# Kernel optimization log

Hardware: AMD Instinct MI355X
Metric: run time of the kernel (lower is better)

The kernel has to match this reference:

```python
import jax, jax.numpy as jnp
import numpy as np

N = 50000   # nodes
E = 800000  # edges (avg degree 16)
IN, H, OUT = 128, 128, 64


def setup_inputs() -> dict:
    key = jax.random.key(0)
    ks = jax.random.split(key, 8)

    def w(k, shape):
        fan_in = shape[0]
        return (jax.random.normal(k, shape, jnp.float32) / np.float32(np.sqrt(fan_in)))

    x = jax.random.normal(ks[0], (N, IN), jnp.float32)
    edge_index = jax.random.randint(ks[1], (2, E), 0, N, jnp.int64)
    return {
        "x": x,
        "edge_index": edge_index,
        "W1": w(ks[2], (IN, H)), "b1": jnp.zeros((H,), jnp.float32),
        "W2": w(ks[3], (H, H)),  "b2": jnp.zeros((H,), jnp.float32),
        "W3": w(ks[4], (H, H)),  "b3": jnp.zeros((H,), jnp.float32),
        "Wd1": w(ks[5], (H, H)), "bd1": jnp.zeros((H,), jnp.float32),
        "Wd2": w(ks[6], (H, OUT)), "bd2": jnp.zeros((OUT,), jnp.float32),
    }


def _gcn_conv(x, src, dst, norm, W, b):
    # x: [N, Cin] -> linear transform, gather along edges, normalized scatter-add
    h = x @ W                                   # [N, Cout]
    msg = h[src] * norm[:, None]                # [E+N, Cout]
    out = jax.ops.segment_sum(msg, dst, num_segments=N)
    return out + b


def reference(x, edge_index, W1, b1, W2, b2, W3, b3, Wd1, bd1, Wd2, bd2):
    # Add self-loops (PyG GCNConv default) and compute symmetric normalization.
    loops = jnp.arange(N, dtype=edge_index.dtype)
    src = jnp.concatenate([edge_index[0], loops])   # [E+N]
    dst = jnp.concatenate([edge_index[1], loops])   # [E+N]
    deg = jax.ops.segment_sum(jnp.ones_like(dst, dtype=x.dtype), dst, num_segments=N)
    dinv = jnp.where(deg > 0, jax.lax.rsqrt(deg), jnp.zeros_like(deg))
    norm = dinv[src] * dinv[dst]                    # [E+N]

    h = jax.nn.relu(_gcn_conv(x, src, dst, norm, W1, b1))
    h = jax.nn.relu(_gcn_conv(h, src, dst, norm, W2, b2))
    h = jax.nn.relu(_gcn_conv(h, src, dst, norm, W3, b3))

    h = jax.nn.relu(h @ Wd1 + bd1)
    return jax.nn.sigmoid(h @ Wd2 + bd2)            # [N, OUT]
```

## Files before the change

kernel.cpp:

```cpp
#include <hip/hip_runtime.h>
#include <hip/hip_bf16.h>
#include <hip/hip_fp16.h>

#define N_NODES 50000
#define N_EDGES 800000
#define C_H 128
#define C_OUT 64
#define NBLK 196
#define TSTRIDE 136
#define E_PAD 950272
#define MM_BLKS 782

typedef __attribute__((ext_vector_type(8))) short bf16x8;
typedef __attribute__((ext_vector_type(4))) float f32x4;

static __device__ __forceinline__ float bf_lo(unsigned int u) { return __uint_as_float(u << 16); }
static __device__ __forceinline__ float bf_hi(unsigned int u) { return __uint_as_float(u & 0xffff0000u); }
static __device__ __forceinline__ unsigned short f2bf(float f) {
    __hip_bfloat16 h = __float2bfloat16(f);
    return *(unsigned short*)&h;
}
static __device__ __forceinline__ unsigned int pack2(float a, float b) {
    return (unsigned int)f2bf(a) | ((unsigned int)f2bf(b) << 16);
}
static __device__ __forceinline__ unsigned short f2h_bits(float f) {
    union { __half h; unsigned short u; } c; c.h = __float2half_rn(f); return c.u;
}
static __device__ __forceinline__ float h_bits2f(unsigned short u) {
    union { __half h; unsigned short u; } c; c.u = u; return __half2float(c.h);
}

__global__ void prep_kernel(const int* __restrict__ dst, int* __restrict__ counts,
                            int* __restrict__ rank,
                            const float* __restrict__ W1, const float* __restrict__ W2,
                            const float* __restrict__ W3, const float* __restrict__ Wd1,
                            const float* __restrict__ Wd2,
                            unsigned short* __restrict__ P1, unsigned short* __restrict__ P2,
                            unsigned short* __restrict__ P3, unsigned short* __restrict__ Pd1,
                            unsigned short* __restrict__ Pd2,
                            unsigned int* __restrict__ epay) {
    int b = blockIdx.x;
    if (b < 3125) {
        int e = b * 256 + threadIdx.x;
        rank[e] = atomicAdd(&counts[dst[e]], 1);
    } else if (b < 3413) {
        int idx = (b - 3125) * 256 + threadIdx.x;
        if (idx < 4 * 16384) {
            int which = idx >> 14;
            int r = idx & 16383;
            const float* W = (which == 0) ? W1 : (which == 1) ? W2 : (which == 2) ? W3 : Wd1;
            unsigned short* P = (which == 0) ? P1 : (which == 1) ? P2 : (which == 2) ? P3 : Pd1;
            int j = r & 7, lane = (r >> 3) & 63, t = r >> 9;
            int nb = t & 7, kb = t >> 3;
            int k = kb * 32 + ((lane >> 4) << 3) + j;
            int n = nb * 16 + (lane & 15);
            P[r] = f2bf(W[(size_t)k * 128 + n]);
        } else {
            int r = idx - 65536;
            if (r < 8192) {
                int j = r & 7, lane = (r >> 3) & 63, t = r >> 9;
                int nb = t & 3, kb = t >> 2;
                int k = kb * 32 + ((lane >> 4) << 3) + j;
                int n = nb * 16 + (lane & 15);
                Pd2[r] = f2bf(Wd2[(size_t)k * 64 + n]);
            }
        }
    } else {
        int i = (b - 3413) * 256 + threadIdx.x;
        *(uint4*)(epay + (size_t)i * 4) = make_uint4(0, 0, 0, 0);
    }
}

__global__ void __launch_bounds__(256) scan_fused_kernel(
        const int* __restrict__ counts, int* __restrict__ bsum, int* __restrict__ bo,
        int* __restrict__ ctr_flag, float* __restrict__ dinv, int* __restrict__ rowptr) {
    __shared__ int ws[4];
    __shared__ int ws2[4];
    __shared__ int sLast;
    const int b = blockIdx.x;
    const int i = b * 256 + threadIdx.x;
    const int lane = threadIdx.x & 63, w = threadIdx.x >> 6;

    int v = (i < N_NODES) ? counts[i] : 0;
    if (i < N_NODES) dinv[i] = rsqrtf((float)v + 1.0f);
    int vp = (v + 3) & ~3;
    int x = vp;
    #pragma unroll
    for (int off = 1; off < 64; off <<= 1) {
        int t = __shfl_up(x, off, 64);
        if (lane >= off) x += t;
    }
    if (lane == 63) ws[w] = x;
    __syncthreads();
    if (threadIdx.x == 0) {
        int run = 0;
        #pragma unroll
        for (int k = 0; k < 4; ++k) { int t = ws[k]; ws[k] = run; run += t; }
        bsum[b] = run;
    }
    __syncthreads();
    int excl_local = x - vp + ws[w];

    if (threadIdx.x == 0) {
        __threadfence();
        int old = __hip_atomic_fetch_add(&ctr_flag[0], 1, __ATOMIC_ACQ_REL, __HIP_MEMORY_SCOPE_AGENT);
        sLast = (old == NBLK - 1) ? 1 : 0;
    }
    __syncthreads();
    if (sLast) {
        int j = threadIdx.x;
        int bv = (j < NBLK) ? bsum[j] : 0;
        int y = bv;
        #pragma unroll
        for (int off = 1; off < 64; off <<= 1) {
            int t = __shfl_up(y, off, 64);
            if (lane >= off) y += t;
        }
        if (lane == 63) ws2[w] = y;
        __syncthreads();
        if (j == 0) {
            int run = 0;
            #pragma unroll
            for (int k = 0; k < 4; ++k) { int t = ws2[k]; ws2[k] = run; run += t; }
        }
        __syncthreads();
        int be = y - bv + ws2[w];
        if (j < NBLK) bo[j] = be;
        if (j == 255) rowptr[N_NODES] = be + bv;
        __syncthreads();
        if (j == 0) {
            __threadfence();
            __hip_atomic_store(&ctr_flag[1], 1, __ATOMIC_RELEASE, __HIP_MEMORY_SCOPE_AGENT);
        }
    }
    if (threadIdx.x == 0) {
        while (__hip_atomic_load(&ctr_flag[1], __ATOMIC_ACQUIRE, __HIP_MEMORY_SCOPE_AGENT) == 0) {}
    }
    __syncthreads();
    if (i < N_NODES) rowptr[i] = excl_local + bo[b];
}

__global__ void __launch_bounds__(256) fill_mm_kernel(
        const float* __restrict__ x, const unsigned short* __restrict__ P1,
        unsigned short* __restrict__ XW1,
        const int* __restrict__ src, const int* __restrict__ dst,
        const float* __restrict__ dinv,
        const int* __restrict__ rowptr, const int* __restrict__ rank,
        unsigned int* __restrict__ epay) {
    int b = blockIdx.x;
    if (b < MM_BLKS) {
        const int lane = threadIdx.x & 63;
        const int wave = threadIdx.x >> 6;
        const int wid  = b * 4 + wave;
        if (wid * 16 >= N_NODES) return;
        const int node = wid * 16 + (lane & 15);
        const int quad = lane >> 4;
        f32x4 acc[8];
        #pragma unroll
        for (int nb = 0; nb < 8; ++nb) acc[nb] = (f32x4){0.f, 0.f, 0.f, 0.f};
        #pragma unroll
        for (int kb = 0; kb < 4; ++kb) {
            const float* p = x + (size_t)node * 128 + kb * 32 + quad * 8;
            float4 lo = *(const float4*)p;
            float4 hi = *(const float4*)(p + 4);
            union { bf16x8 v; unsigned int u[4]; } tmp;
            tmp.u[0] = pack2(lo.x, lo.y); tmp.u[1] = pack2(lo.z, lo.w);
            tmp.u[2] = pack2(hi.x, hi.y); tmp.u[3] = pack2(hi.z, hi.w);
            #pragma unroll
            for (int nb = 0; nb < 8; ++nb) {
                bf16x8 wf = *(const bf16x8*)(P1 + ((size_t)(kb * 8 + nb) * 64 + lane) * 8);
                acc[nb] = __builtin_amdgcn_mfma_f32_16x16x32_bf16(wf, tmp.v, acc[nb], 0, 0, 0);
            }
        }
        #pragma unroll
        for (int nb = 0; nb < 8; ++nb) {
            int ch = nb * 16 + quad * 4;
            uint2 o;
            o.x = pack2(acc[nb][0], acc[nb][1]);
            o.y = pack2(acc[nb][2], acc[nb][3]);
            *(uint2*)(XW1 + (size_t)node * C_H + ch) = o;
        }
    } else {
        int e = (b - MM_BLKS) * 256 + threadIdx.x;
        if (e < N_EDGES) {
            int d = dst[e], s = src[e];
            int pos = rowptr[d] + rank[e];
            float nrm = dinv[s] * dinv[d];
            epay[pos] = (unsigned int)s | ((unsigned int)f2h_bits(nrm) << 16);
        }
    }
}

static __device__ __forceinline__ void gather_row(
        const unsigned int* __restrict__ epay,
        const unsigned short* __restrict__ hin,
        int beg, int end, int c8, float dii, uint4 selfraw, float* a) {
    a[0] = bf_lo(selfraw.x) * dii; a[1] = bf_hi(selfraw.x) * dii;
    a[2] = bf_lo(selfraw.y) * dii; a[3] = bf_hi(selfraw.y) * dii;
    a[4] = bf_lo(selfraw.z) * dii; a[5] = bf_hi(selfraw.z) * dii;
    a[6] = bf_lo(selfraw.w) * dii; a[7] = bf_hi(selfraw.w) * dii;
    int p = beg;
    for (; p + 8 <= end; p += 8) {
        uint4 ev0 = *(const uint4*)(epay + p);
        uint4 ev1 = *(const uint4*)(epay + p + 4);
        unsigned int ee[8] = {ev0.x, ev0.y, ev0.z, ev0.w, ev1.x, ev1.y, ev1.z, ev1.w};
        uint4 rv[8];
        #pragma unroll
        for (int j = 0; j < 8; ++j)
            rv[j] = *(const uint4*)(hin + (size_t)(ee[j] & 0xffffu) * C_H + c8);
        #pragma unroll
        for (int j = 0; j < 8; ++j) {
            float nm = h_bits2f((unsigned short)(ee[j] >> 16));
            a[0] = fmaf(bf_lo(rv[j].x), nm, a[0]); a[1] = fmaf(bf_hi(rv[j].x), nm, a[1]);
            a[2] = fmaf(bf_lo(rv[j].y), nm, a[2]); a[3] = fmaf(bf_hi(rv[j].y), nm, a[3]);
            a[4] = fmaf(bf_lo(rv[j].z), nm, a[4]); a[5] = fmaf(bf_hi(rv[j].z), nm, a[5]);
            a[6] = fmaf(bf_lo(rv[j].w), nm, a[6]); a[7] = fmaf(bf_hi(rv[j].w), nm, a[7]);
        }
    }
    if (p < end) {
        uint4 ev = *(const uint4*)(epay + p);
        unsigned int ee[4] = {ev.x, ev.y, ev.z, ev.w};
        uint4 rv[4];
        #pragma unroll
        for (int j = 0; j < 4; ++j)
            rv[j] = *(const uint4*)(hin + (size_t)(ee[j] & 0xffffu) * C_H + c8);
        #pragma unroll
        for (int j = 0; j < 4; ++j) {
            float nm = h_bits2f((unsigned short)(ee[j] >> 16));
            a[0] = fmaf(bf_lo(rv[j].x), nm, a[0]); a[1] = fmaf(bf_hi(rv[j].x), nm, a[1]);
            a[2] = fmaf(bf_lo(rv[j].y), nm, a[2]); a[3] = fmaf(bf_hi(rv[j].y), nm, a[3]);
            a[4] = fmaf(bf_lo(rv[j].z), nm, a[4]); a[5] = fmaf(bf_hi(rv[j].z), nm, a[5]);
            a[6] = fmaf(bf_lo(rv[j].w), nm, a[6]); a[7] = fmaf(bf_hi(rv[j].w), nm, a[7]);
        }
    }
}

__global__ void __launch_bounds__(256) gather1_kernel(
        const int* __restrict__ rowptr,
        const unsigned int* __restrict__ epay,
        const float* __restrict__ dinv,
        const unsigned short* __restrict__ hin,
        const float* __restrict__ bias,
        unsigned short* __restrict__ out) {
    int t    = blockIdx.x * 256 + threadIdx.x;
    int node = t >> 4;
    int c8   = (t & 15) << 3;

    float di = dinv[node];
    uint4 raw = *(const uint4*)(hin + (size_t)node * C_H + c8);
    float a[8];
    gather_row(epay, hin, rowptr[node], rowptr[node + 1], c8, di * di, raw, a);

    float4 ba = *(const float4*)(bias + c8);
    float4 bb = *(const float4*)(bias + c8 + 4);
    a[0] = fmaxf(a[0] + ba.x, 0.f); a[1] = fmaxf(a[1] + ba.y, 0.f);
    a[2] = fmaxf(a[2] + ba.z, 0.f); a[3] = fmaxf(a[3] + ba.w, 0.f);
    a[4] = fmaxf(a[4] + bb.x, 0.f); a[5] = fmaxf(a[5] + bb.y, 0.f);
    a[6] = fmaxf(a[6] + bb.z, 0.f); a[7] = fmaxf(a[7] + bb.w, 0.f);
    uint4 o;
    o.x = pack2(a[0], a[1]); o.y = pack2(a[2], a[3]);
    o.z = pack2(a[4], a[5]); o.w = pack2(a[6], a[7]);
    *(uint4*)(out + (size_t)node * C_H + c8) = o;
}

template <bool FINAL>
__global__ void __launch_bounds__(256) fused_layer_kernel(
        const int* __restrict__ rowptr,
        const unsigned int* __restrict__ epay,
        const float* __restrict__ dinv,
        const unsigned short* __restrict__ hin,
        const unsigned short* __restrict__ Wp,
        const float* __restrict__ bias,
        const unsigned short* __restrict__ Wd1p,
        const float* __restrict__ bd1,
        const unsigned short* __restrict__ Wd2p,
        const float* __restrict__ bd2,
        unsigned short* __restrict__ out_b,
        float* __restrict__ out_f) {
    __shared__ unsigned short sG[16 * TSTRIDE];
    const int t = threadIdx.x;

    {
        int nl = t >> 4, c8 = (t & 15) << 3;
        int nd = blockIdx.x * 16 + nl;
        float di = dinv[nd];
        uint4 raw = *(const uint4*)(hin + (size_t)nd * C_H + c8);
        float a[8];
        gather_row(epay, hin, rowptr[nd], rowptr[nd + 1], c8, di * di, raw, a);
        uint4 o;
        o.x = pack2(a[0], a[1]); o.y = pack2(a[2], a[3]);
        o.z = pack2(a[4], a[5]); o.w = pack2(a[6], a[7]);
        *(uint4*)(sG + nl * TSTRIDE + c8) = o;
    }
    __syncthreads();

    const int lane = t & 63, wave = t >> 6, quad = lane >> 4, row = lane & 15;
    const int node = blockIdx.x * 16 + row;

    f32x4 acc0 = (f32x4){0.f, 0.f, 0.f, 0.f};
    f32x4 acc1 = (f32x4){0.f, 0.f, 0.f, 0.f};
    const int nb0 = 2 * wave, nb1 = 2 * wave + 1;
    #pragma unroll
    for (int kb = 0; kb < 4; ++kb) {
        bf16x8 hf = *(const bf16x8*)(sG + row * TSTRIDE + kb * 32 + quad * 8);
        bf16x8 wf0 = *(const bf16x8*)(Wp + ((size_t)(kb * 8 + nb0) * 64 + lane) * 8);
        bf16x8 wf1 = *(const bf16x8*)(Wp + ((size_t)(kb * 8 + nb1) * 64 + lane) * 8);
        acc0 = __builtin_amdgcn_mfma_f32_16x16x32_bf16(wf0, hf, acc0, 0, 0, 0);
        acc1 = __builtin_amdgcn_mfma_f32_16x16x32_bf16(wf1, hf, acc1, 0, 0, 0);
    }
    float4 ba0 = *(const float4*)(bias + nb0 * 16 + quad * 4);
    float4 ba1 = *(const float4*)(bias + nb1 * 16 + quad * 4);
    float v00 = fmaxf(acc0[0] + ba0.x, 0.f), v01 = fmaxf(acc0[1] + ba0.y, 0.f);
    float v02 = fmaxf(acc0[2] + ba0.z, 0.f), v03 = fmaxf(acc0[3] + ba0.w, 0.f);
    float v10 = fmaxf(acc1[0] + ba1.x, 0.f), v11 = fmaxf(acc1[1] + ba1.y, 0.f);
    float v12 = fmaxf(acc1[2] + ba1.z, 0.f), v13 = fmaxf(acc1[3] + ba1.w, 0.f);

    if (!FINAL) {
        uint2 o0, o1;
        o0.x = pack2(v00, v01); o0.y = pack2(v02, v03);
        o1.x = pack2(v10, v11); o1.y = pack2(v12, v13);
        *(uint2*)(out_b + (size_t)node * C_H + nb0 * 16 + quad * 4) = o0;
        *(uint2*)(out_b + (size_t)node * C_H + nb1 * 16 + quad * 4) = o1;
        return;
    }

    __syncthreads();
    {
        uint2 o0, o1;
        o0.x = pack2(v00, v01); o0.y = pack2(v02, v03);
        o1.x = pack2(v10, v11); o1.y = pack2(v12, v13);
        *(uint2*)(sG + row * TSTRIDE + nb0 * 16 + quad * 4) = o0;
        *(uint2*)(sG + row * TSTRIDE + nb1 * 16 + quad * 4) = o1;
    }
    __syncthreads();

    acc0 = (f32x4){0.f, 0.f, 0.f, 0.f};
    acc1 = (f32x4){0.f, 0.f, 0.f, 0.f};
    #pragma unroll
    for (int kb = 0; kb < 4; ++kb) {
        bf16x8 hf = *(const bf16x8*)(sG + row * TSTRIDE + kb * 32 + quad * 8);
        bf16x8 wf0 = *(const bf16x8*)(Wd1p + ((size_t)(kb * 8 + nb0) * 64 + lane) * 8);
        bf16x8 wf1 = *(const bf16x8*)(Wd1p + ((size_t)(kb * 8 + nb1) * 64 + lane) * 8);
        acc0 = __builtin_amdgcn_mfma_f32_16x16x32_bf16(wf0, hf, acc0, 0, 0, 0);
        acc1 = __builtin_amdgcn_mfma_f32_16x16x32_bf16(wf1, hf, acc1, 0, 0, 0);
    }
    ba0 = *(const float4*)(bd1 + nb0 * 16 + quad * 4);
    ba1 = *(const float4*)(bd1 + nb1 * 16 + quad * 4);
    v00 = fmaxf(acc0[0] + ba0.x, 0.f); v01 = fmaxf(acc0[1] + ba0.y, 0.f);
    v02 = fmaxf(acc0[2] + ba0.z, 0.f); v03 = fmaxf(acc0[3] + ba0.w, 0.f);
    v10 = fmaxf(acc1[0] + ba1.x, 0.f); v11 = fmaxf(acc1[1] + ba1.y, 0.f);
    v12 = fmaxf(acc1[2] + ba1.z, 0.f); v13 = fmaxf(acc1[3] + ba1.w, 0.f);
    __syncthreads();
    {
        uint2 o0, o1;
        o0.x = pack2(v00, v01); o0.y = pack2(v02, v03);
        o1.x = pack2(v10, v11); o1.y = pack2(v12, v13);
        *(uint2*)(sG + row * TSTRIDE + nb0 * 16 + quad * 4) = o0;
        *(uint2*)(sG + row * TSTRIDE + nb1 * 16 + quad * 4) = o1;
    }
    __syncthreads();

    f32x4 acc = (f32x4){0.f, 0.f, 0.f, 0.f};
    #pragma unroll
    for (int kb = 0; kb < 4; ++kb) {
        bf16x8 hf = *(const bf16x8*)(sG + row * TSTRIDE + kb * 32 + quad * 8);
        bf16x8 wf = *(const bf16x8*)(Wd2p + ((size_t)(kb * 4 + wave) * 64 + lane) * 8);
        acc = __builtin_amdgcn_mfma_f32_16x16x32_bf16(wf, hf, acc, 0, 0, 0);
    }
    int ch = wave * 16 + quad * 4;
    float4 b4 = *(const float4*)(bd2 + ch);
    float4 r;
    r.x = 1.f / (1.f + expf(-(acc[0] + b4.x)));
    r.y = 1.f / (1.f + expf(-(acc[1] + b4.y)));
    r.z = 1.f / (1.f + expf(-(acc[2] + b4.z)));
    r.w = 1.f / (1.f + expf(-(acc[3] + b4.w)));
    *(float4*)(out_f + (size_t)node * C_OUT + ch) = r;
}

extern "C" void kernel_launch(void* const* d_in, const int* in_sizes, int n_in,
                              void* d_out, int out_size, void* d_ws, size_t ws_size,
                              hipStream_t stream) {
    const float* x   = (const float*)d_in[0];
    const int*   ei  = (const int*)d_in[1];
    const float* W1  = (const float*)d_in[2];
    const float* b1  = (const float*)d_in[3];
    const float* W2  = (const float*)d_in[4];
    const float* b2  = (const float*)d_in[5];
    const float* W3  = (const float*)d_in[6];
    const float* b3  = (const float*)d_in[7];
    const float* Wd1 = (const float*)d_in[8];
    const float* bd1 = (const float*)d_in[9];
    const float* Wd2 = (const float*)d_in[10];
    const float* bd2 = (const float*)d_in[11];

    const int* src = ei;
    const int* dst = ei + N_EDGES;

    char* base = (char*)d_ws;
    size_t off = 0;
    auto alloc = [&](size_t bytes) { char* p = base + off; off += (bytes + 255) & ~size_t(255); return p; };
    int*            counts = (int*)alloc(50176 * 4);
    unsigned int*   epay   = (unsigned int*)alloc((size_t)E_PAD * 4);
    int*            rank   = (int*)alloc((size_t)N_EDGES * 4);
    float*          dinv   = (float*)alloc(N_NODES * 4);
    int*            rowptr = (int*)alloc((N_NODES + 1) * 4);
    int*            bsum   = (int*)alloc(256 * 4);
    int*            bo     = (int*)alloc(256 * 4);
    unsigned short* XW1    = (unsigned short*)alloc((size_t)N_NODES * C_H * 2);
    unsigned short* bufA   = (unsigned short*)alloc((size_t)N_NODES * C_H * 2);
    unsigned short* bufB   = (unsigned short*)alloc((size_t)N_NODES * C_H * 2);
    unsigned short* P1     = (unsigned short*)alloc(128 * 128 * 2);
    unsigned short* P2     = (unsigned short*)alloc(128 * 128 * 2);
    unsigned short* P3     = (unsigned short*)alloc(128 * 128 * 2);
    unsigned short* Pd1    = (unsigned short*)alloc(128 * 128 * 2);
    unsigned short* Pd2    = (unsigned short*)alloc(128 * 64 * 2);
    int* ctr_flag = counts + 50100;

    const int T = 256;
    dim3 blk(T);
    dim3 gPrep(3125 + 288 + E_PAD / 1024);
    dim3 gScan(NBLK);
    dim3 gFillMM(MM_BLKS + 3125);
    dim3 gFused(N_NODES / 16);

    hipMemsetAsync(counts, 0, 50176 * 4, stream);
    prep_kernel<<<gPrep, blk, 0, stream>>>(dst, counts, rank,
                                           W1, W2, W3, Wd1, Wd2,
                                           P1, P2, P3, Pd1, Pd2, epay);
    scan_fused_kernel<<<gScan, blk, 0, stream>>>(counts, bsum, bo, ctr_flag, dinv, rowptr);
    fill_mm_kernel<<<gFillMM, blk, 0, stream>>>(x, P1, XW1, src, dst, dinv,
                                                rowptr, rank, epay);

    gather1_kernel<<<gFused, blk, 0, stream>>>(rowptr, epay, dinv, XW1, b1, bufA);
    fused_layer_kernel<false><<<gFused, blk, 0, stream>>>(
        rowptr, epay, dinv, bufA, P2, b2, nullptr, nullptr, nullptr, nullptr, bufB, nullptr);
    fused_layer_kernel<true><<<gFused, blk, 0, stream>>>(
        rowptr, epay, dinv, bufB, P3, b3, Pd1, bd1, Pd2, bd2, nullptr, (float*)d_out);
}
```

Baseline: 265.5 us.

## Sort nodes by degree bucket to balance gather work across waves

Builds a degree-bucketed node permutation: a per-block 64-bin degree histogram, a global column scan across blocks, and a scatter into a perm array. The gather and fused layer kernels then process nodes in that order so that the 16 nodes sharing a block have similar edge counts, which is meant to cut divergence and tail imbalance in the neighbour loops. The single-kernel scan with its spin-wait is replaced by three kernels, which adds launches and a serial per-column loop in a one-block kernel. Output rows become non-contiguous per block, which may hurt write coalescing and locality.

```diff
diff --git a/kernel.cpp b/kernel.cpp
--- a/kernel.cpp
+++ b/kernel.cpp
@@ -71,19 +71,20 @@
     }
 }
 
-__global__ void __launch_bounds__(256) scan_fused_kernel(
-        const int* __restrict__ counts, int* __restrict__ bsum, int* __restrict__ bo,
-        int* __restrict__ ctr_flag, float* __restrict__ dinv, int* __restrict__ rowptr) {
+__global__ void __launch_bounds__(256) scan1_kernel(const int* __restrict__ counts,
+                                                    int* __restrict__ eblk,
+                                                    int* __restrict__ bsum,
+                                                    float* __restrict__ dinv,
+                                                    int* __restrict__ dtemp,
+                                                    int* __restrict__ bhist) {
     __shared__ int ws[4];
-    __shared__ int ws2[4];
-    __shared__ int sLast;
-    const int b = blockIdx.x;
-    const int i = b * 256 + threadIdx.x;
-    const int lane = threadIdx.x & 63, w = threadIdx.x >> 6;
-
+    __shared__ int h[64];
+    if (threadIdx.x < 64) h[threadIdx.x] = 0;
+    int i = blockIdx.x * 256 + threadIdx.x;
     int v = (i < N_NODES) ? counts[i] : 0;
     if (i < N_NODES) dinv[i] = rsqrtf((float)v + 1.0f);
     int vp = (v + 3) & ~3;
+    int lane = threadIdx.x & 63, w = threadIdx.x >> 6;
     int x = vp;
     #pragma unroll
     for (int off = 1; off < 64; off <<= 1) {
@@ -92,52 +93,76 @@
     }
     if (lane == 63) ws[w] = x;
     __syncthreads();
+    if (i < N_NODES) {
+        int bin = min(v, 63);
+        dtemp[i] = atomicAdd(&h[bin], 1);
+    }
     if (threadIdx.x == 0) {
         int run = 0;
         #pragma unroll
         for (int k = 0; k < 4; ++k) { int t = ws[k]; ws[k] = run; run += t; }
-        bsum[b] = run;
-    }
-    __syncthreads();
-    int excl_local = x - vp + ws[w];
-
-    if (threadIdx.x == 0) {
-        __threadfence();
-        int old = __hip_atomic_fetch_add(&ctr_flag[0], 1, __ATOMIC_ACQ_REL, __HIP_MEMORY_SCOPE_AGENT);
-        sLast = (old == NBLK - 1) ? 1 : 0;
-    }
-    __syncthreads();
-    if (sLast) {
+        bsum[blockIdx.x] = run;
+    }
+    __syncthreads();
+    if (i < N_NODES) eblk[i] = x - vp + ws[w];
+    if (threadIdx.x < 64) bhist[blockIdx.x * 64 + threadIdx.x] = h[threadIdx.x];
+}
+
+__global__ void __launch_bounds__(256) scan2_kernel(const int* __restrict__ bsum,
+                                                    int* __restrict__ bo,
+                                                    int* __restrict__ rowptr,
+                                                    int* __restrict__ bhist) {
+    __shared__ int ws[4];
+    int i = threadIdx.x;
+    int v = (i < NBLK) ? bsum[i] : 0;
+    int lane = i & 63, w = i >> 6;
+    int x = v;
+    #pragma unroll
+    for (int off = 1; off < 64; off <<= 1) {
+        int t = __shfl_up(x, off, 64);
+        if (lane >= off) x += t;
+    }
+    if (lane == 63) ws[w] = x;
+    __syncthreads();
+    if (i == 0) {
+        int run = 0;
+        #pragma unroll
+        for (int k = 0; k < 4; ++k) { int t = ws[k]; ws[k] = run; run += t; }
+    }
+    __syncthreads();
+    int excl = x - v + ws[w];
+    if (i < NBLK) bo[i] = excl;
+    if (i == 255) rowptr[N_NODES] = excl + v;
+
+    if (threadIdx.x < 64) {
         int j = threadIdx.x;
-        int bv = (j < NBLK) ? bsum[j] : 0;
-        int y = bv;
+        int run = 0;
+        for (int b = 0; b < NBLK; ++b) {
+            int t = bhist[b * 64 + j];
+            bhist[b * 64 + j] = run;
+            run += t;
+        }
+        int x2 = run;
         #pragma unroll
         for (int off = 1; off < 64; off <<= 1) {
-            int t = __shfl_up(y, off, 64);
-            if (lane >= off) y += t;
-        }
-        if (lane == 63) ws2[w] = y;
-        __syncthreads();
-        if (j == 0) {
-            int run = 0;
-            #pragma unroll
-            for (int k = 0; k < 4; ++k) { int t = ws2[k]; ws2[k] = run; run += t; }
-        }
-        __syncthreads();
-        int be = y - bv + ws2[w];
-        if (j < NBLK) bo[j] = be;
-        if (j == 255) rowptr[N_NODES] = be + bv;
-        __syncthreads();
-        if (j == 0) {
-            __threadfence();
-            __hip_atomic_store(&ctr_flag[1], 1, __ATOMIC_RELEASE, __HIP_MEMORY_SCOPE_AGENT);
-        }
-    }
-    if (threadIdx.x == 0) {
-        while (__hip_atomic_load(&ctr_flag[1], __ATOMIC_ACQUIRE, __HIP_MEMORY_SCOPE_AGENT) == 0) {}
-    }
-    __syncthreads();
-    if (i < N_NODES) rowptr[i] = excl_local + bo[b];
+            int t = __shfl_up(x2, off, 64);
+            if (j >= off) x2 += t;
+        }
+        int base = x2 - run;
+        for (int b = 0; b < NBLK; ++b) bhist[b * 64 + j] += base;
+    }
+}
+
+__global__ void scan3_kernel(const int* __restrict__ eblk, const int* __restrict__ bo,
+                             int* __restrict__ rowptr,
+                             const int* __restrict__ counts, const int* __restrict__ dtemp,
+                             const int* __restrict__ bhist, int* __restrict__ perm) {
+    int i = blockIdx.x * 256 + threadIdx.x;
+    if (i < N_NODES) {
+        rowptr[i] = eblk[i] + bo[blockIdx.x];
+        int bin = min(counts[i], 63);
+        perm[bhist[blockIdx.x * 64 + bin] + dtemp[i]] = i;
+    }
 }
 
 __global__ void __launch_bounds__(256) fill_mm_kernel(
@@ -239,11 +264,12 @@
         const int* __restrict__ rowptr,
         const unsigned int* __restrict__ epay,
         const float* __restrict__ dinv,
+        const int* __restrict__ perm,
         const unsigned short* __restrict__ hin,
         const float* __restrict__ bias,
         unsigned short* __restrict__ out) {
     int t    = blockIdx.x * 256 + threadIdx.x;
-    int node = t >> 4;
+    int node = perm[t >> 4];
     int c8   = (t & 15) << 3;
 
     float di = dinv[node];
@@ -268,6 +294,7 @@
         const int* __restrict__ rowptr,
         const unsigned int* __restrict__ epay,
         const float* __restrict__ dinv,
+        const int* __restrict__ perm,
         const unsigned short* __restrict__ hin,
         const unsigned short* __restrict__ Wp,
         const float* __restrict__ bias,
@@ -282,7 +309,7 @@
 
     {
         int nl = t >> 4, c8 = (t & 15) << 3;
-        int nd = blockIdx.x * 16 + nl;
+        int nd = perm[blockIdx.x * 16 + nl];
         float di = dinv[nd];
         uint4 raw = *(const uint4*)(hin + (size_t)nd * C_H + c8);
         float a[8];
@@ -295,7 +322,7 @@
     __syncthreads();
 
     const int lane = t & 63, wave = t >> 6, quad = lane >> 4, row = lane & 15;
-    const int node = blockIdx.x * 16 + row;
+    const int node = perm[blockIdx.x * 16 + row];
 
     f32x4 acc0 = (f32x4){0.f, 0.f, 0.f, 0.f};
     f32x4 acc1 = (f32x4){0.f, 0.f, 0.f, 0.f};
@@ -404,8 +431,12 @@
     int*            rank   = (int*)alloc((size_t)N_EDGES * 4);
     float*          dinv   = (float*)alloc(N_NODES * 4);
     int*            rowptr = (int*)alloc((N_NODES + 1) * 4);
+    int*            eblk   = (int*)alloc(N_NODES * 4);
     int*            bsum   = (int*)alloc(256 * 4);
     int*            bo     = (int*)alloc(256 * 4);
+    int*            dtemp  = (int*)alloc(N_NODES * 4);
+    int*            bhist  = (int*)alloc(NBLK * 64 * 4);
+    int*            perm   = (int*)alloc(N_NODES * 4);
     unsigned short* XW1    = (unsigned short*)alloc((size_t)N_NODES * C_H * 2);
     unsigned short* bufA   = (unsigned short*)alloc((size_t)N_NODES * C_H * 2);
     unsigned short* bufB   = (unsigned short*)alloc((size_t)N_NODES * C_H * 2);
@@ -414,12 +445,11 @@
     unsigned short* P3     = (unsigned short*)alloc(128 * 128 * 2);
     unsigned short* Pd1    = (unsigned short*)alloc(128 * 128 * 2);
     unsigned short* Pd2    = (unsigned short*)alloc(128 * 64 * 2);
-    int* ctr_flag = counts + 50100;
 
     const int T = 256;
     dim3 blk(T);
+    dim3 gN((N_NODES + T - 1) / T);
     dim3 gPrep(3125 + 288 + E_PAD / 1024);
-    dim3 gScan(NBLK);
     dim3 gFillMM(MM_BLKS + 3125);
     dim3 gFused(N_NODES / 16);
 
@@ -427,13 +457,15 @@
     prep_kernel<<<gPrep, blk, 0, stream>>>(dst, counts, rank,
                                            W1, W2, W3, Wd1, Wd2,
                                            P1, P2, P3, Pd1, Pd2, epay);
-    scan_fused_kernel<<<gScan, blk, 0, stream>>>(counts, bsum, bo, ctr_flag, dinv, rowptr);
+    scan1_kernel<<<gN, blk, 0, stream>>>(counts, eblk, bsum, dinv, dtemp, bhist);
+    scan2_kernel<<<1, blk, 0, stream>>>(bsum, bo, rowptr, bhist);
+    scan3_kernel<<<gN, blk, 0, stream>>>(eblk, bo, rowptr, counts, dtemp, bhist, perm);
     fill_mm_kernel<<<gFillMM, blk, 0, stream>>>(x, P1, XW1, src, dst, dinv,
                                                 rowptr, rank, epay);
 
-    gather1_kernel<<<gFused, blk, 0, stream>>>(rowptr, epay, dinv, XW1, b1, bufA);
+    gather1_kernel<<<gFused, blk, 0, stream>>>(rowptr, epay, dinv, perm, XW1, b1, bufA);
     fused_layer_kernel<false><<<gFused, blk, 0, stream>>>(
-        rowptr, epay, dinv, bufA, P2, b2, nullptr, nullptr, nullptr, nullptr, bufB, nullptr);
+        rowptr, epay, dinv, perm, bufA, P2, b2, nullptr, nullptr, nullptr, nullptr, bufB, nullptr);
     fused_layer_kernel<true><<<gFused, blk, 0, stream>>>(
-        rowptr, epay, dinv, bufB, P3, b3, Pd1, bd1, Pd2, bd2, nullptr, (float*)d_out);
-}
+        rowptr, epay, dinv, perm, bufB, P3, b3, Pd1, bd1, Pd2, bd2, nullptr, (float*)d_out);
+}
```

Result: slower. 271.8 us (+2.4%).
